# Performance work log

Measured on AMD Instinct MI355X. Metric: run time of the kernel, lower is better.

The kernel has to match this reference:

```python
import jax, jax.numpy as jnp
import numpy as np

RADIUS = 3       # corr_radius
NUM_LEVELS = 4   # corr_lvls


def avg_pool2(x):
    """2x2 avg-pool with stride 2 on the last two axes (floor semantics, like F.avg_pool2d)."""
    nd = x.ndim
    s = jax.lax.reduce_window(
        x, 0.0, jax.lax.add,
        window_dimensions=(1,) * (nd - 2) + (2, 2),
        window_strides=(1,) * (nd - 2) + (2, 2),
        padding='VALID')
    return s * 0.25


def bilinear_window_lookup(corr, coords, radius):
    """corr: [B,H,W,hl,wl] per-pixel correlation maps; coords: [B,H,W,2] (x,y) in
    level-pixel units. Samples a (2r+1)^2 window around each coord with bilinear
    interpolation and zero padding (matches grid_sample align_corners=True, zeros).
    Returns [B,H,W,(2r+1)^2]."""
    B, H, W, hl, wl = corr.shape
    r = radius
    d = jnp.arange(-r, r + 1, dtype=coords.dtype)
    dy, dx = jnp.meshgrid(d, d, indexing='ij')
    delta = jnp.stack([dx.ravel(), dy.ravel()], axis=-1)        # [K2,2] (x,y)
    pts = coords[:, :, :, None, :] + delta                       # [B,H,W,K2,2]
    x, y = pts[..., 0], pts[..., 1]
    x0 = jnp.floor(x); y0 = jnp.floor(y)
    x1 = x0 + 1.0;     y1 = y0 + 1.0
    wx1 = x - x0; wx0 = 1.0 - wx1
    wy1 = y - y0; wy0 = 1.0 - wy1
    bi = jnp.arange(B)[:, None, None, None]
    hi = jnp.arange(H)[None, :, None, None]
    wi = jnp.arange(W)[None, None, :, None]

    def gather(xc, yc):
        valid = (xc >= 0) & (xc <= wl - 1) & (yc >= 0) & (yc <= hl - 1)
        xi = jnp.clip(xc, 0, wl - 1).astype(jnp.int32)
        yi = jnp.clip(yc, 0, hl - 1).astype(jnp.int32)
        return corr[bi, hi, wi, yi, xi] * valid.astype(corr.dtype)

    return (gather(x0, y0) * wx0 * wy0 + gather(x1, y0) * wx1 * wy0 +
            gather(x0, y1) * wx0 * wy1 + gather(x1, y1) * wx1 * wy1)


def pyramid_lookup(pyr, coords, radius):
    """pyr: list of [B,H,W,hl,wl]; coords: [B,H,W,2] at full level-0 resolution.
    Returns [B, L*(2r+1)^2, H, W]."""
    outs = [bilinear_window_lookup(c, coords / float(2 ** lvl), radius)
            for lvl, c in enumerate(pyr)]
    out = jnp.concatenate(outs, axis=-1)
    return jnp.transpose(out, (0, 3, 1, 2))


def setup_inputs() -> dict:
    key = jax.random.key(0)
    k0, k1, k2, k3, k4 = jax.random.split(key, 5)
    B, D, H, W = 1, 128, 60, 108  # 1/8-res features of a padded 480x864 frame
    fmap0 = jax.random.normal(k0, (B, D, H, W), dtype=jnp.float32)
    fmap1 = jax.random.normal(k1, (B, D, H, W), dtype=jnp.float32)
    flow0 = jax.random.normal(k2, (B, 2, H, W), dtype=jnp.float32)
    flow1 = jax.random.normal(k3, (B, 2, H, W), dtype=jnp.float32)
    embt = jax.random.uniform(k4, (B, 1, 1, 1), dtype=jnp.float32,
                              minval=0.1, maxval=0.9)
    return {"fmap0": fmap0, "fmap1": fmap1, "flow0": flow0,
            "flow1": flow1, "embt": embt}


def reference(fmap0, fmap1, flow0, flow1, embt):
    """BidirCorrBlock construction + AMT._corr_scale_lookup (downsample=1).
    Returns [B, 2*L*(2r+1)^2 + 4, H, W]: bidirectional multi-level correlation
    features concatenated with the stacked flows (corr, flow of the torch code)."""
    B, D, H, W = fmap0.shape
    # all-pairs correlation volume, scaled by 1/sqrt(D) as in RAFT's CorrBlock
    corr = jnp.einsum('bchw,bcuv->bhwuv', fmap0, fmap1) / jnp.sqrt(
        jnp.asarray(D, fmap0.dtype))                       # [B,H,W,H,W]
    corr_T = jnp.transpose(corr, (0, 3, 4, 1, 2))          # reversed direction
    pyr, pyr_T = [corr], [corr_T]
    for _ in range(NUM_LEVELS - 1):
        pyr.append(avg_pool2(pyr[-1]))
        pyr_T.append(avg_pool2(pyr_T[-1]))

    # coords_grid: channels (x, y)
    ys, xs = jnp.meshgrid(jnp.arange(H, dtype=fmap0.dtype),
                          jnp.arange(W, dtype=fmap0.dtype), indexing='ij')
    coord = jnp.broadcast_to(jnp.stack([xs, ys], axis=-1), (B, H, W, 2))

    t1_scale = 1.0 / embt           # [B,1,1,1]
    t0_scale = 1.0 / (1.0 - embt)
    f0 = jnp.transpose(flow0, (0, 2, 3, 1))  # [B,H,W,2]
    f1 = jnp.transpose(flow1, (0, 2, 3, 1))
    coords0 = coord + f1 * t1_scale          # lookup args of corr_fn(...)
    coords1 = coord + f0 * t0_scale

    corr0 = pyramid_lookup(pyr, coords0, RADIUS)     # [B, L*K2, H, W]
    corr1 = pyramid_lookup(pyr_T, coords1, RADIUS)
    corr_out = jnp.concatenate([corr0, corr1], axis=1)
    flow_out = jnp.concatenate([flow0, flow1], axis=1)
    return jnp.concatenate([corr_out, flow_out], axis=1)
```

## Files before the change

### kernel.cpp

```cpp
#include <hip/hip_runtime.h>

typedef _Float16 h16;
typedef __attribute__((ext_vector_type(2))) h16 h2v;
typedef __attribute__((ext_vector_type(8))) h16 h8v;

constexpr int H_ = 60, W_ = 108, HW_ = 6480;

constexpr unsigned B_F0T  = 0;
constexpr unsigned B_F1T  = 1658880;
constexpr unsigned B_F0L1 = 3317760;
constexpr unsigned B_F0L2 = 3732480;
constexpr unsigned B_F0L3 = 3836160;
constexpr unsigned B_F1L1 = 3859456;
constexpr unsigned B_F1L2 = 4274176;
constexpr unsigned B_F1L3 = 4377856;

__global__ __launch_bounds__(256) void k_transpose(const float* __restrict__ f0,
                                                   const float* __restrict__ f1,
                                                   h16* __restrict__ ws) {
    __shared__ float lds[64 * 129];
    const float* src = blockIdx.y ? f1 : f0;
    h16* dst = (h16*)((char*)ws + (blockIdx.y ? B_F1T : B_F0T));
    const int p0 = blockIdx.x * 64;
    const int t  = threadIdx.x;
    const int pr = t & 63, cr = t >> 6;
    #pragma unroll
    for (int cb = 0; cb < 128; cb += 4) {
        int c = cb + cr, p = p0 + pr;
        if (p < HW_) lds[pr * 129 + c] = src[(size_t)c * HW_ + p];
    }
    __syncthreads();
    const float S = 0.29730177875068026f;
    const int cw = t & 63, pw = t >> 6;
    #pragma unroll
    for (int pb = 0; pb < 64; pb += 4) {
        int p = p0 + pb + pw;
        if (p < HW_) {
            float a = lds[(pb + pw) * 129 + 2 * cw] * S;
            float b = lds[(pb + pw) * 129 + 2 * cw + 1] * S;
            h2v v; v.x = (h16)a; v.y = (h16)b;
            ((h2v*)dst)[(size_t)p * 64 + cw] = v;
        }
    }
}

__global__ __launch_bounds__(256) void k_pyramid(h16* __restrict__ wsh) {
    char* ws = (char*)wsh;
    const int map = blockIdx.y;
    const char* s = ws + (map ? B_F1T : B_F0T);
    const int bid = blockIdx.x;
    const int t = threadIdx.x;

    if (bid < 102) {
        const int idx = bid * 256 + t;
        if (idx >= 1620 * 16) return;
        const int pos = idx >> 4, q = idx & 15;
        const int y = pos / 54, x = pos - y * 54;
        const unsigned r0 = (unsigned)(2 * y * 108 + 2 * x) * 256 + q * 16;
        const unsigned r1 = r0 + 108 * 256;
        h8v a = *(const h8v*)(s + r0);
        h8v b = *(const h8v*)(s + r0 + 256);
        h8v c = *(const h8v*)(s + r1);
        h8v d = *(const h8v*)(s + r1 + 256);
        h8v o;
        #pragma unroll
        for (int k = 0; k < 8; ++k)
            o[k] = (h16)((((float)a[k] + (float)b[k]) + ((float)c[k] + (float)d[k])) * 0.25f);
        *(h8v*)(ws + (map ? B_F1L1 : B_F0L1) + (unsigned)pos * 256 + q * 16) = o;
    } else if (bid < 128) {
        const int idx = (bid - 102) * 256 + t;
        if (idx >= 405 * 16) return;
        const int pos = idx >> 4, q = idx & 15;
        const int y = pos / 27, x = pos - y * 27;
        float acc[8] = {};
        #pragma unroll
        for (int dy = 0; dy < 4; ++dy) {
            #pragma unroll
            for (int dx = 0; dx < 4; ++dx) {
                h8v u = *(const h8v*)(s + (unsigned)((4 * y + dy) * 108 + 4 * x + dx) * 256 + q * 16);
                #pragma unroll
                for (int k = 0; k < 8; ++k) acc[k] += (float)u[k];
            }
        }
        h8v o;
        #pragma unroll
        for (int k = 0; k < 8; ++k) o[k] = (h16)(acc[k] * 0.0625f);
        *(h8v*)(ws + (map ? B_F1L2 : B_F0L2) + (unsigned)pos * 256 + q * 16) = o;
    } else {
        const int idx = (bid - 128) * 256 + t;
        if (idx >= 91 * 128) return;
        const int pos = idx >> 7;
        const int sub = idx & 127;
        const int half = sub >> 6, lane = sub & 63;
        const int j = lane >> 3, qq = (lane & 7) + half * 8;
        const int y = pos / 13, x = pos - y * 13;
        float acc[8] = {};
        #pragma unroll
        for (int dx = 0; dx < 8; ++dx) {
            h8v u = *(const h8v*)(s + (unsigned)((8 * y + j) * 108 + 8 * x + dx) * 256 + qq * 16);
            #pragma unroll
            for (int k = 0; k < 8; ++k) acc[k] += (float)u[k];
        }
        #pragma unroll
        for (int k = 0; k < 8; ++k) {
            acc[k] += __shfl_xor(acc[k], 8);
            acc[k] += __shfl_xor(acc[k], 16);
            acc[k] += __shfl_xor(acc[k], 32);
        }
        if (j == 0) {
            h8v o;
            #pragma unroll
            for (int k = 0; k < 8; ++k) o[k] = (h16)(acc[k] * 0.015625f);
            *(h8v*)(ws + (map ? B_F1L3 : B_F0L3) + (unsigned)pos * 256 + qq * 16) = o;
        }
    }
}

template <int CTRL>
__device__ __forceinline__ float dpp_add(float x) {
    int y = __builtin_amdgcn_update_dpp(0, __builtin_bit_cast(int, x),
                                        CTRL, 0xF, 0xF, true);
    return x + __builtin_bit_cast(float, y);
}

__device__ __forceinline__ float dot_u4(uint4 u, uint4 s, float acc) {
    acc = __builtin_amdgcn_fdot2(__builtin_bit_cast(h2v, u.x),
                                 __builtin_bit_cast(h2v, s.x), acc, false);
    acc = __builtin_amdgcn_fdot2(__builtin_bit_cast(h2v, u.y),
                                 __builtin_bit_cast(h2v, s.y), acc, false);
    acc = __builtin_amdgcn_fdot2(__builtin_bit_cast(h2v, u.z),
                                 __builtin_bit_cast(h2v, s.z), acc, false);
    acc = __builtin_amdgcn_fdot2(__builtin_bit_cast(h2v, u.w),
                                 __builtin_bit_cast(h2v, s.w), acc, false);
    return acc;
}

__global__ __launch_bounds__(256, 4) void k_lookup(const h16* __restrict__ wsh,
                                                   const float* __restrict__ flow0,
                                                   const float* __restrict__ flow1,
                                                   const float* __restrict__ embt,
                                                   float* __restrict__ out) {
    __shared__ float so[196][5];
    __shared__ char l3cache[91 * 256];
    const char* ws = (const char*)wsh;
    const int bid = blockIdx.x;
    const int xcd = bid & 7;
    const int dir = xcd >> 2;
    const int ord = (xcd & 3) * 405 + (bid >> 3);
    const int pix0 = ord * 4;
    const int t = threadIdx.x;
    const int L = t & 63;
    const int pix = pix0 + (t >> 6);
    const int h = pix / 108, w = pix - h * 108;

    {
        const char* l3src = ws + (dir ? B_F0L3 : B_F1L3);
        #pragma unroll
        for (int i = 0; i < 6; ++i) {
            const int c = t + i * 256;
            if (c < 91 * 16)
                ((uint4*)l3cache)[c] = *(const uint4*)(l3src + c * 16);
        }
    }

    const float e = embt[0];
    const float scale = dir ? 1.0f / (1.0f - e) : 1.0f / e;
    const float* fl = dir ? flow0 : flow1;
    const float cx = (float)w + fl[pix] * scale;
    const float cy = (float)h + fl[HW_ + pix] * scale;

    const int ch = L & 7;
    const int p  = L >> 3;

    const unsigned sbase = (dir ? B_F1T : B_F0T) + (unsigned)pix * 256;
    const uint4 su0 = *(const uint4*)(ws + sbase + ch * 16);
    const uint4 su1 = *(const uint4*)(ws + sbase + 128 + ch * 16);

    constexpr unsigned g0[4] = {B_F1T, B_F1L1, B_F1L2, B_F1L3};
    constexpr unsigned g1[4] = {B_F0T, B_F0L1, B_F0L2, B_F0L3};

    __syncthreads();

    #pragma unroll
    for (int lvl = 0; lvl < 4; ++lvl) {
        const unsigned gbase = dir ? g1[lvl] : g0[lvl];
        const int wl = 108 >> lvl, hl = 60 >> lvl;
        const float inv = (lvl == 0) ? 1.f : (lvl == 1) ? 0.5f : (lvl == 2) ? 0.25f : 0.125f;
        const float cxl = cx * inv, cyl = cy * inv;
        const float bxf = floorf(cxl), byf = floorf(cyl);
        const int bx = (int)bxf, by = (int)byf;
        const int gx = bx - 3 + p;
        const int gxc = min(max(gx, 0), wl - 1);
        const bool colv = (gx >= 0) & (gx < wl);
        const int gyo = by - 3 + ch;
        const bool ownv = colv & (gyo >= 0) & (gyo < hl);

        uint4 u0[8], u1[8];
        if (lvl == 3) {
            const unsigned co = (unsigned)gxc * 256 + (unsigned)ch * 16;
            #pragma unroll
            for (int j = 0; j < 8; ++j) {
                const int gy = by - 3 + j;
                const int gyc = min(max(gy, 0), hl - 1);
                const unsigned ro = co + (unsigned)(gyc * wl) * 256;
                u0[j] = *(const uint4*)(l3cache + ro);
                u1[j] = *(const uint4*)(l3cache + ro + 128);
            }
        } else {
            const unsigned coloff = gbase + (unsigned)gxc * 256 + (unsigned)ch * 16;
            #pragma unroll
            for (int j = 0; j < 8; ++j) {
                const int gy = by - 3 + j;
                const int gyc = min(max(gy, 0), hl - 1);
                const unsigned ro = coloff + (unsigned)(gyc * wl) * 256;
                u0[j] = *(const uint4*)(ws + ro);
                u1[j] = *(const uint4*)(ws + ro + 128);
            }
        }

        float dval = 0.0f;
        #pragma unroll
        for (int j = 0; j < 8; ++j) {
            float a0 = dot_u4(u0[j], su0, 0.0f);
            float a1 = dot_u4(u1[j], su1, 0.0f);
            float acc = a0 + a1;
            acc = dpp_add<0xB1>(acc);
            acc = dpp_add<0x4E>(acc);
            acc = dpp_add<0x141>(acc);
            dval = (ch == j) ? acc : dval;
        }
        dval = ownv ? dval : 0.0f;

        const int dyi = L / 7, dxi = L - dyi * 7;
        const float fx = cxl - bxf, fy = cyl - byf;
        const float d00 = __shfl(dval, 8 * dxi + dyi);
        const float d01 = __shfl(dval, 8 * dxi + dyi + 8);
        const float d10 = __shfl(dval, 8 * dxi + dyi + 1);
        const float d11 = __shfl(dval, 8 * dxi + dyi + 9);
        const float v = (d00 * (1.0f - fx) + d01 * fx) * (1.0f - fy) +
                        (d10 * (1.0f - fx) + d11 * fx) * fy;
        if (L < 49) so[lvl * 49 + L][t >> 6] = v;
    }
    __syncthreads();

    if (t < 196) {
        float4 o = make_float4(so[t][0], so[t][1], so[t][2], so[t][3]);
        *(float4*)(out + (size_t)(dir * 196 + t) * HW_ + pix0) = o;
    } else if (dir == 0 && t < 200) {
        const int c = t - 196;
        const float* f = (c < 2) ? flow0 + (size_t)c * HW_
                                 : flow1 + (size_t)(c - 2) * HW_;
        *(float4*)(out + (size_t)(392 + c) * HW_ + pix0) = *(const float4*)(f + pix0);
    }
}

extern "C" void kernel_launch(void* const* d_in, const int* in_sizes, int n_in,
                              void* d_out, int out_size, void* d_ws, size_t ws_size,
                              hipStream_t stream) {
    const float* fmap0 = (const float*)d_in[0];
    const float* fmap1 = (const float*)d_in[1];
    const float* flow0 = (const float*)d_in[2];
    const float* flow1 = (const float*)d_in[3];
    const float* embt  = (const float*)d_in[4];
    h16* ws  = (h16*)d_ws;
    float* out = (float*)d_out;

    k_transpose<<<dim3(102, 2), 256, 0, stream>>>(fmap0, fmap1, ws);
    k_pyramid<<<dim3(174, 2), 256, 0, stream>>>(ws);
    k_lookup<<<dim3(405 * 8), 256, 0, stream>>>(ws, flow0, flow1, embt, out);
}
```

Baseline: 42.06 us.

## Use persistent lookup blocks caching pyramid levels 2 and 3 in shared memory

Replaces the 3240-block lookup grid with 256 persistent 512-thread blocks. Each block stages both coarse pyramid levels (2 and 3) into about 124 KB of dynamic LDS once, then loops over groups of 4 pixels per wavefront, with each wave writing its outputs directly. The aim is to amortise the LDS staging over many pixels and to serve level-2 gathers from LDS instead of global memory. The cost is occupancy: with so much LDS per block only one block fits per CU, and the grid covers at most 256 CUs with uneven per-block row counts. Per-pixel work is now serialized inside each wave, so latency hiding depends on the per-wave unrolled loads.

```diff
diff --git a/kernel.cpp b/kernel.cpp
--- a/kernel.cpp
+++ b/kernel.cpp
@@ -135,122 +135,140 @@
     return acc;
 }
 
-__global__ __launch_bounds__(256, 4) void k_lookup(const h16* __restrict__ wsh,
-                                                   const float* __restrict__ flow0,
-                                                   const float* __restrict__ flow1,
-                                                   const float* __restrict__ embt,
-                                                   float* __restrict__ out) {
-    __shared__ float so[196][5];
-    __shared__ char l3cache[91 * 256];
+__global__ __launch_bounds__(512, 2) void k_lookup2(const h16* __restrict__ wsh,
+                                                    const float* __restrict__ flow0,
+                                                    const float* __restrict__ flow1,
+                                                    const float* __restrict__ embt,
+                                                    float* __restrict__ out) {
+    extern __shared__ char lds2[];
     const char* ws = (const char*)wsh;
     const int bid = blockIdx.x;
     const int xcd = bid & 7;
     const int dir = xcd >> 2;
-    const int ord = (xcd & 3) * 405 + (bid >> 3);
-    const int pix0 = ord * 4;
+    const int dirblk = (bid >> 3) * 4 + (xcd & 3);
     const int t = threadIdx.x;
     const int L = t & 63;
-    const int pix = pix0 + (t >> 6);
-    const int h = pix / 108, w = pix - h * 108;
+    const int wv = t >> 6;
 
     {
-        const char* l3src = ws + (dir ? B_F0L3 : B_F1L3);
-        #pragma unroll
-        for (int i = 0; i < 6; ++i) {
-            const int c = t + i * 256;
-            if (c < 91 * 16)
-                ((uint4*)l3cache)[c] = *(const uint4*)(l3src + c * 16);
+        const uint4* src = (const uint4*)(ws + (dir ? B_F0L2 : B_F1L2));
+        #pragma unroll
+        for (int i = 0; i < 16; ++i) {
+            const int c = t + i * 512;
+            if (c < 7936) ((uint4*)lds2)[c] = src[c];
         }
     }
 
     const float e = embt[0];
     const float scale = dir ? 1.0f / (1.0f - e) : 1.0f / e;
     const float* fl = dir ? flow0 : flow1;
-    const float cx = (float)w + fl[pix] * scale;
-    const float cy = (float)h + fl[HW_ + pix] * scale;
+    const unsigned sB  = dir ? B_F1T : B_F0T;
+    const unsigned gB0 = dir ? B_F0T : B_F1T;
+    const unsigned gB1 = dir ? B_F0L1 : B_F1L1;
 
     const int ch = L & 7;
     const int p  = L >> 3;
 
-    const unsigned sbase = (dir ? B_F1T : B_F0T) + (unsigned)pix * 256;
-    const uint4 su0 = *(const uint4*)(ws + sbase + ch * 16);
-    const uint4 su1 = *(const uint4*)(ws + sbase + 128 + ch * 16);
-
-    constexpr unsigned g0[4] = {B_F1T, B_F1L1, B_F1L2, B_F1L3};
-    constexpr unsigned g1[4] = {B_F0T, B_F0L1, B_F0L2, B_F0L3};
-
     __syncthreads();
 
-    #pragma unroll
-    for (int lvl = 0; lvl < 4; ++lvl) {
-        const unsigned gbase = dir ? g1[lvl] : g0[lvl];
-        const int wl = 108 >> lvl, hl = 60 >> lvl;
-        const float inv = (lvl == 0) ? 1.f : (lvl == 1) ? 0.5f : (lvl == 2) ? 0.25f : 0.125f;
-        const float cxl = cx * inv, cyl = cy * inv;
-        const float bxf = floorf(cxl), byf = floorf(cyl);
-        const int bx = (int)bxf, by = (int)byf;
-        const int gx = bx - 3 + p;
-        const int gxc = min(max(gx, 0), wl - 1);
-        const bool colv = (gx >= 0) & (gx < wl);
-        const int gyo = by - 3 + ch;
-        const bool ownv = colv & (gyo >= 0) & (gyo < hl);
-
-        uint4 u0[8], u1[8];
-        if (lvl == 3) {
-            const unsigned co = (unsigned)gxc * 256 + (unsigned)ch * 16;
-            #pragma unroll
-            for (int j = 0; j < 8; ++j) {
-                const int gy = by - 3 + j;
-                const int gyc = min(max(gy, 0), hl - 1);
-                const unsigned ro = co + (unsigned)(gyc * wl) * 256;
-                u0[j] = *(const uint4*)(l3cache + ro);
-                u1[j] = *(const uint4*)(l3cache + ro + 128);
+    const int rbeg = (dirblk * 1620) >> 7;
+    const int rend = ((dirblk + 1) * 1620) >> 7;
+
+    for (int r = rbeg + wv; r < rend; r += 8) {
+        const int px0 = r * 4;
+
+        float cxa[4], cya[4];
+        uint4 su0a[4], su1a[4];
+        #pragma unroll
+        for (int pp = 0; pp < 4; ++pp) {
+            const int pix = px0 + pp;
+            const int hh = pix / 108, ww = pix - hh * 108;
+            cxa[pp] = (float)ww + fl[pix] * scale;
+            cya[pp] = (float)hh + fl[HW_ + pix] * scale;
+            const unsigned sbase = sB + (unsigned)pix * 256;
+            su0a[pp] = *(const uint4*)(ws + sbase + ch * 16);
+            su1a[pp] = *(const uint4*)(ws + sbase + 128 + ch * 16);
+        }
+
+        float vals[4][4];
+        #pragma unroll
+        for (int pp = 0; pp < 4; ++pp) {
+            const float cx = cxa[pp], cy = cya[pp];
+            const uint4 su0 = su0a[pp], su1 = su1a[pp];
+            #pragma unroll
+            for (int lvl = 0; lvl < 4; ++lvl) {
+                const int wl = 108 >> lvl, hl = 60 >> lvl;
+                const float inv = (lvl == 0) ? 1.f : (lvl == 1) ? 0.5f
+                                : (lvl == 2) ? 0.25f : 0.125f;
+                const float cxl = cx * inv, cyl = cy * inv;
+                const float bxf = floorf(cxl), byf = floorf(cyl);
+                const int bx = (int)bxf, by = (int)byf;
+                const int gx = bx - 3 + p;
+                const int gxc = min(max(gx, 0), wl - 1);
+                const bool colv = (gx >= 0) & (gx < wl);
+                const int gyo = by - 3 + ch;
+                const bool ownv = colv & (gyo >= 0) & (gyo < hl);
+
+                uint4 u0[8], u1[8];
+                if (lvl >= 2) {
+                    const char* base = (lvl == 3) ? (lds2 + 103680) : lds2;
+                    const unsigned co = (unsigned)gxc * 256 + (unsigned)ch * 16;
+                    #pragma unroll
+                    for (int j = 0; j < 8; ++j) {
+                        const int gy = by - 3 + j;
+                        const int gyc = min(max(gy, 0), hl - 1);
+                        const unsigned ro = co + (unsigned)(gyc * wl) * 256;
+                        u0[j] = *(const uint4*)(base + ro);
+                        u1[j] = *(const uint4*)(base + ro + 128);
+                    }
+                } else {
+                    const unsigned gbase = (lvl == 0) ? gB0 : gB1;
+                    const unsigned coloff = gbase + (unsigned)gxc * 256 + (unsigned)ch * 16;
+                    #pragma unroll
+                    for (int j = 0; j < 8; ++j) {
+                        const int gy = by - 3 + j;
+                        const int gyc = min(max(gy, 0), hl - 1);
+                        const unsigned ro = coloff + (unsigned)(gyc * wl) * 256;
+                        u0[j] = *(const uint4*)(ws + ro);
+                        u1[j] = *(const uint4*)(ws + ro + 128);
+                    }
+                }
+
+                float dval = 0.0f;
+                #pragma unroll
+                for (int j = 0; j < 8; ++j) {
+                    float a0 = dot_u4(u0[j], su0, 0.0f);
+                    float a1 = dot_u4(u1[j], su1, 0.0f);
+                    float acc = a0 + a1;
+                    acc = dpp_add<0xB1>(acc);
+                    acc = dpp_add<0x4E>(acc);
+                    acc = dpp_add<0x141>(acc);
+                    dval = (ch == j) ? acc : dval;
+                }
+                dval = ownv ? dval : 0.0f;
+
+                const int dyi = L / 7, dxi = L - dyi * 7;
+                const float fx = cxl - bxf, fy = cyl - byf;
+                const float d00 = __shfl(dval, 8 * dxi + dyi);
+                const float d01 = __shfl(dval, 8 * dxi + dyi + 8);
+                const float d10 = __shfl(dval, 8 * dxi + dyi + 1);
+                const float d11 = __shfl(dval, 8 * dxi + dyi + 9);
+                vals[lvl][pp] = (d00 * (1.0f - fx) + d01 * fx) * (1.0f - fy) +
+                                (d10 * (1.0f - fx) + d11 * fx) * fy;
             }
-        } else {
-            const unsigned coloff = gbase + (unsigned)gxc * 256 + (unsigned)ch * 16;
-            #pragma unroll
-            for (int j = 0; j < 8; ++j) {
-                const int gy = by - 3 + j;
-                const int gyc = min(max(gy, 0), hl - 1);
-                const unsigned ro = coloff + (unsigned)(gyc * wl) * 256;
-                u0[j] = *(const uint4*)(ws + ro);
-                u1[j] = *(const uint4*)(ws + ro + 128);
-            }
-        }
-
-        float dval = 0.0f;
-        #pragma unroll
-        for (int j = 0; j < 8; ++j) {
-            float a0 = dot_u4(u0[j], su0, 0.0f);
-            float a1 = dot_u4(u1[j], su1, 0.0f);
-            float acc = a0 + a1;
-            acc = dpp_add<0xB1>(acc);
-            acc = dpp_add<0x4E>(acc);
-            acc = dpp_add<0x141>(acc);
-            dval = (ch == j) ? acc : dval;
-        }
-        dval = ownv ? dval : 0.0f;
-
-        const int dyi = L / 7, dxi = L - dyi * 7;
-        const float fx = cxl - bxf, fy = cyl - byf;
-        const float d00 = __shfl(dval, 8 * dxi + dyi);
-        const float d01 = __shfl(dval, 8 * dxi + dyi + 8);
-        const float d10 = __shfl(dval, 8 * dxi + dyi + 1);
-        const float d11 = __shfl(dval, 8 * dxi + dyi + 9);
-        const float v = (d00 * (1.0f - fx) + d01 * fx) * (1.0f - fy) +
-                        (d10 * (1.0f - fx) + d11 * fx) * fy;
-        if (L < 49) so[lvl * 49 + L][t >> 6] = v;
-    }
-    __syncthreads();
-
-    if (t < 196) {
-        float4 o = make_float4(so[t][0], so[t][1], so[t][2], so[t][3]);
-        *(float4*)(out + (size_t)(dir * 196 + t) * HW_ + pix0) = o;
-    } else if (dir == 0 && t < 200) {
-        const int c = t - 196;
-        const float* f = (c < 2) ? flow0 + (size_t)c * HW_
-                                 : flow1 + (size_t)(c - 2) * HW_;
-        *(float4*)(out + (size_t)(392 + c) * HW_ + pix0) = *(const float4*)(f + pix0);
+        }
+
+        #pragma unroll
+        for (int lvl = 0; lvl < 4; ++lvl)
+            if (L < 49)
+                *(float4*)(out + (size_t)(dir * 196 + lvl * 49 + L) * HW_ + px0) =
+                    make_float4(vals[lvl][0], vals[lvl][1], vals[lvl][2], vals[lvl][3]);
+        if (dir == 0 && L >= 49 && L < 53) {
+            const int c = L - 49;
+            const float* f = (c < 2) ? flow0 + (size_t)c * HW_
+                                     : flow1 + (size_t)(c - 2) * HW_;
+            *(float4*)(out + (size_t)(392 + c) * HW_ + px0) = *(const float4*)(f + px0);
+        }
     }
 }
 
@@ -265,7 +283,10 @@
     h16* ws  = (h16*)d_ws;
     float* out = (float*)d_out;
 
+    (void)hipFuncSetAttribute((const void*)k_lookup2,
+                              hipFuncAttributeMaxDynamicSharedMemorySize, 126976);
+
     k_transpose<<<dim3(102, 2), 256, 0, stream>>>(fmap0, fmap1, ws);
     k_pyramid<<<dim3(174, 2), 256, 0, stream>>>(ws);
-    k_lookup<<<dim3(405 * 8), 256, 0, stream>>>(ws, flow0, flow1, embt, out);
-}
+    k_lookup2<<<dim3(256), 512, 126976, stream>>>(ws, flow0, flow1, embt, out);
+}
```

After: 45.65 us. 8.5% more time.

## Fuse feature transpose and pooled pyramid build into one tiled kernel

Applied to the files above, without the earlier changes.

Merges the transpose/scale kernel and the pyramid pooling kernel into a single kernel that loads an 8x8 spatial tile of all 128 channels into LDS, writes the level-0 fp16 features, and computes levels 1-3 from the tile. This removes one kernel launch and the global re-read of level-0 data for pooling. Level-3 is computed by 16 threads looping serially over 64 positions, and the fp32 load is now strided per channel with less coalescing (8-wide rows), which may cost bandwidth and leave the tail of each block underused.

```diff
diff --git a/kernel.cpp b/kernel.cpp
--- a/kernel.cpp
+++ b/kernel.cpp
@@ -15,104 +15,96 @@
 constexpr unsigned B_F1L2 = 4274176;
 constexpr unsigned B_F1L3 = 4377856;
 
-__global__ __launch_bounds__(256) void k_transpose(const float* __restrict__ f0,
-                                                   const float* __restrict__ f1,
-                                                   h16* __restrict__ ws) {
-    __shared__ float lds[64 * 129];
-    const float* src = blockIdx.y ? f1 : f0;
-    h16* dst = (h16*)((char*)ws + (blockIdx.y ? B_F1T : B_F0T));
-    const int p0 = blockIdx.x * 64;
-    const int t  = threadIdx.x;
-    const int pr = t & 63, cr = t >> 6;
-    #pragma unroll
-    for (int cb = 0; cb < 128; cb += 4) {
-        int c = cb + cr, p = p0 + pr;
-        if (p < HW_) lds[pr * 129 + c] = src[(size_t)c * HW_ + p];
-    }
-    __syncthreads();
-    const float S = 0.29730177875068026f;
-    const int cw = t & 63, pw = t >> 6;
-    #pragma unroll
-    for (int pb = 0; pb < 64; pb += 4) {
-        int p = p0 + pb + pw;
-        if (p < HW_) {
-            float a = lds[(pb + pw) * 129 + 2 * cw] * S;
-            float b = lds[(pb + pw) * 129 + 2 * cw + 1] * S;
-            h2v v; v.x = (h16)a; v.y = (h16)b;
-            ((h2v*)dst)[(size_t)p * 64 + cw] = v;
-        }
-    }
-}
-
-__global__ __launch_bounds__(256) void k_pyramid(h16* __restrict__ wsh) {
+__global__ __launch_bounds__(256) void k_prep(const float* __restrict__ f0,
+                                              const float* __restrict__ f1,
+                                              h16* __restrict__ wsh) {
+    __shared__ h16 tile[64 * 136];
     char* ws = (char*)wsh;
     const int map = blockIdx.y;
-    const char* s = ws + (map ? B_F1T : B_F0T);
-    const int bid = blockIdx.x;
+    const float* src = map ? f1 : f0;
+    const unsigned oL0 = map ? B_F1T  : B_F0T;
+    const unsigned oL1 = map ? B_F1L1 : B_F0L1;
+    const unsigned oL2 = map ? B_F1L2 : B_F0L2;
+    const unsigned oL3 = map ? B_F1L3 : B_F0L3;
+    const int tx = blockIdx.x % 14, ty = blockIdx.x / 14;
+    const int x0 = tx * 8, y0 = ty * 8;
+    const int tw = min(8, 108 - x0), th = min(8, 60 - y0);
     const int t = threadIdx.x;
-
-    if (bid < 102) {
-        const int idx = bid * 256 + t;
-        if (idx >= 1620 * 16) return;
-        const int pos = idx >> 4, q = idx & 15;
-        const int y = pos / 54, x = pos - y * 54;
-        const unsigned r0 = (unsigned)(2 * y * 108 + 2 * x) * 256 + q * 16;
-        const unsigned r1 = r0 + 108 * 256;
-        h8v a = *(const h8v*)(s + r0);
-        h8v b = *(const h8v*)(s + r0 + 256);
-        h8v c = *(const h8v*)(s + r1);
-        h8v d = *(const h8v*)(s + r1 + 256);
+    const float S = 0.29730177875068026f;
+
+    {
+        const int L = t & 63, c0 = t >> 6;
+        const int lx = L & 7, ly = L >> 3;
+        const int gx = min(x0 + lx, 107), gy = min(y0 + ly, 59);
+        const int gpos = gy * 108 + gx;
+        #pragma unroll
+        for (int k = 0; k < 32; ++k) {
+            const int c = c0 * 32 + k;
+            tile[L * 136 + c] = (h16)(src[(size_t)c * 6480 + gpos] * S);
+        }
+    }
+    __syncthreads();
+
+    #pragma unroll
+    for (int i = 0; i < 4; ++i) {
+        const int u = t + i * 256;
+        const int pos = u >> 4, q = u & 15;
+        const int plx = pos & 7, ply = pos >> 3;
+        if (plx < tw && ply < th) {
+            h8v v = *(const h8v*)&tile[pos * 136 + q * 8];
+            *(h8v*)(ws + oL0 + (unsigned)((y0 + ply) * 108 + x0 + plx) * 256 + q * 16) = v;
+        }
+    }
+    {
+        const int pos = t >> 4, q = t & 15;
+        const int px = pos & 3, py = pos >> 2;
+        if (px < (tw >> 1) && py < (th >> 1)) {
+            float a[8] = {};
+            #pragma unroll
+            for (int dy = 0; dy < 2; ++dy)
+                #pragma unroll
+                for (int dx = 0; dx < 2; ++dx) {
+                    h8v v = *(const h8v*)&tile[((2*py+dy)*8 + 2*px+dx) * 136 + q * 8];
+                    #pragma unroll
+                    for (int k = 0; k < 8; ++k) a[k] += (float)v[k];
+                }
+            h8v o;
+            #pragma unroll
+            for (int k = 0; k < 8; ++k) o[k] = (h16)(a[k] * 0.25f);
+            *(h8v*)(ws + oL1 + (unsigned)((y0/2 + py) * 54 + x0/2 + px) * 256 + q * 16) = o;
+        }
+    }
+    if (t < 64) {
+        const int pos = t >> 4, q = t & 15;
+        const int px = pos & 1, py = pos >> 1;
+        if (px < (tw >> 2) && py < (th >> 2)) {
+            float a[8] = {};
+            #pragma unroll
+            for (int dy = 0; dy < 4; ++dy)
+                #pragma unroll
+                for (int dx = 0; dx < 4; ++dx) {
+                    h8v v = *(const h8v*)&tile[((4*py+dy)*8 + 4*px+dx) * 136 + q * 8];
+                    #pragma unroll
+                    for (int k = 0; k < 8; ++k) a[k] += (float)v[k];
+                }
+            h8v o;
+            #pragma unroll
+            for (int k = 0; k < 8; ++k) o[k] = (h16)(a[k] * 0.0625f);
+            *(h8v*)(ws + oL2 + (unsigned)((y0/4 + py) * 27 + x0/4 + px) * 256 + q * 16) = o;
+        }
+    }
+    if (t < 16 && tx < 13 && ty < 7) {
+        const int q = t;
+        float a[8] = {};
+        for (int pos = 0; pos < 64; ++pos) {
+            h8v v = *(const h8v*)&tile[pos * 136 + q * 8];
+            #pragma unroll
+            for (int k = 0; k < 8; ++k) a[k] += (float)v[k];
+        }
         h8v o;
         #pragma unroll
-        for (int k = 0; k < 8; ++k)
-            o[k] = (h16)((((float)a[k] + (float)b[k]) + ((float)c[k] + (float)d[k])) * 0.25f);
-        *(h8v*)(ws + (map ? B_F1L1 : B_F0L1) + (unsigned)pos * 256 + q * 16) = o;
-    } else if (bid < 128) {
-        const int idx = (bid - 102) * 256 + t;
-        if (idx >= 405 * 16) return;
-        const int pos = idx >> 4, q = idx & 15;
-        const int y = pos / 27, x = pos - y * 27;
-        float acc[8] = {};
-        #pragma unroll
-        for (int dy = 0; dy < 4; ++dy) {
-            #pragma unroll
-            for (int dx = 0; dx < 4; ++dx) {
-                h8v u = *(const h8v*)(s + (unsigned)((4 * y + dy) * 108 + 4 * x + dx) * 256 + q * 16);
-                #pragma unroll
-                for (int k = 0; k < 8; ++k) acc[k] += (float)u[k];
-            }
-        }
-        h8v o;
-        #pragma unroll
-        for (int k = 0; k < 8; ++k) o[k] = (h16)(acc[k] * 0.0625f);
-        *(h8v*)(ws + (map ? B_F1L2 : B_F0L2) + (unsigned)pos * 256 + q * 16) = o;
-    } else {
-        const int idx = (bid - 128) * 256 + t;
-        if (idx >= 91 * 128) return;
-        const int pos = idx >> 7;
-        const int sub = idx & 127;
-        const int half = sub >> 6, lane = sub & 63;
-        const int j = lane >> 3, qq = (lane & 7) + half * 8;
-        const int y = pos / 13, x = pos - y * 13;
-        float acc[8] = {};
-        #pragma unroll
-        for (int dx = 0; dx < 8; ++dx) {
-            h8v u = *(const h8v*)(s + (unsigned)((8 * y + j) * 108 + 8 * x + dx) * 256 + qq * 16);
-            #pragma unroll
-            for (int k = 0; k < 8; ++k) acc[k] += (float)u[k];
-        }
-        #pragma unroll
-        for (int k = 0; k < 8; ++k) {
-            acc[k] += __shfl_xor(acc[k], 8);
-            acc[k] += __shfl_xor(acc[k], 16);
-            acc[k] += __shfl_xor(acc[k], 32);
-        }
-        if (j == 0) {
-            h8v o;
-            #pragma unroll
-            for (int k = 0; k < 8; ++k) o[k] = (h16)(acc[k] * 0.015625f);
-            *(h8v*)(ws + (map ? B_F1L3 : B_F0L3) + (unsigned)pos * 256 + qq * 16) = o;
-        }
+        for (int k = 0; k < 8; ++k) o[k] = (h16)(a[k] * 0.015625f);
+        *(h8v*)(ws + oL3 + (unsigned)(ty * 13 + tx) * 256 + q * 16) = o;
     }
 }
 
@@ -265,7 +257,6 @@
     h16* ws  = (h16*)d_ws;
     float* out = (float*)d_out;
 
-    k_transpose<<<dim3(102, 2), 256, 0, stream>>>(fmap0, fmap1, ws);
-    k_pyramid<<<dim3(174, 2), 256, 0, stream>>>(ws);
+    k_prep<<<dim3(112, 2), 256, 0, stream>>>(fmap0, fmap1, ws);
     k_lookup<<<dim3(405 * 8), 256, 0, stream>>>(ws, flow0, flow1, embt, out);
 }
```

Measured after the change: 43.37 us. 1.03x slower.
